# Performance work log

Measured on AMD Instinct MI355X. Metric: run time of the kernel, lower is better.

## Reference

```python
import jax, jax.numpy as jnp
import numpy as np

EPS = 1e-5
B, CIN, L = 512, 5, 1024   # batch, input channels, msp length == d_model
COUT, A, NB = 32, 13, 5    # CNN branch channels, max_atoms, num_bonds_prediction


def conv1d(x, w, pad, groups=1):
    # x: (N, C, L), w: (O, I/groups, K)
    return jax.lax.conv_general_dilated(
        x, w, window_strides=(1,), padding=[(pad, pad)],
        dimension_numbers=("NCH", "OIH", "NCH"), feature_group_count=groups)


def batchnorm(x, g, b):
    # training-mode BN over (N, L) per channel, as nn.BatchNorm1d in train()
    m = jnp.mean(x, axis=(0, 2), keepdims=True)
    v = jnp.var(x, axis=(0, 2), keepdims=True)
    return (x - m) * jax.lax.rsqrt(v + EPS) * g[None, :, None] + b[None, :, None]


def setup_inputs() -> dict:
    key = jax.random.key(0)
    ks = jax.random.split(key, 16)
    n = jax.random.normal
    inp = {
        "src": n(ks[0], (B, CIN, L), dtype=jnp.float32),
        "mask": jnp.ones((B, A), dtype=bool),
        "max_atoms": A,
        # CNN branch 1 (kernel 5) : depthwise, pointwise, BN, residual 1x1 conv
        "dw1": n(ks[1], (CIN, 1, 5), dtype=jnp.float32) * 0.2,
        "pw1": n(ks[2], (COUT, CIN, 1), dtype=jnp.float32) * 0.2,
        "g1": jnp.ones((COUT,), jnp.float32),
        "be1": jnp.zeros((COUT,), jnp.float32),
        "r1w": n(ks[3], (COUT, CIN, 1), dtype=jnp.float32) * 0.2,
        "r1b": jnp.zeros((COUT,), jnp.float32),
        # CNN branch 2 (kernel 3)
        "dw2": n(ks[4], (CIN, 1, 3), dtype=jnp.float32) * 0.2,
        "pw2": n(ks[5], (COUT, CIN, 1), dtype=jnp.float32) * 0.2,
        "g2": jnp.ones((COUT,), jnp.float32),
        "be2": jnp.zeros((COUT,), jnp.float32),
        "r2w": n(ks[6], (COUT, CIN, 1), dtype=jnp.float32) * 0.2,
        "r2b": jnp.zeros((COUT,), jnp.float32),
        # EdgeClassify2 linears: ll1 (2*COUT -> A), fl (2*L -> NB)
        "ll1w": n(ks[7], (A, 2 * COUT), dtype=jnp.float32) * 0.1,
        "ll1b": jnp.zeros((A,), jnp.float32),
        "flw": n(ks[8], (NB, 2 * L), dtype=jnp.float32) * 0.02,
        "flb": jnp.zeros((NB,), jnp.float32),
    }
    return inp


def reference(src, mask, max_atoms, dw1, pw1, g1, be1, r1w, r1b,
              dw2, pw2, g2, be2, r2w, r2b, ll1w, ll1b, flw, flb):
    # ---- CNN encoder ----
    e1 = jax.nn.relu(batchnorm(conv1d(conv1d(src, dw1, 2, groups=CIN), pw1, 0), g1, be1))
    e1 = e1 * (conv1d(src, r1w, 0) + r1b[None, :, None])
    e2 = jax.nn.relu(batchnorm(conv1d(conv1d(src, dw2, 1, groups=CIN), pw2, 0), g2, be2))
    e2 = e2 * (conv1d(src, r2w, 0) + r2b[None, :, None])
    x = jnp.concatenate([e1, e2], axis=1)          # (B, 2*COUT, L)
    # ---- EdgeClassify2 ----
    # ll1 over channel dim: (B, 2*COUT, L) -> (B, A, L)
    h = jnp.einsum("bcl,ac->bal", x, ll1w) + ll1b[None, :, None]
    # vectorized replacement of the O(A^2) python loop:
    # final_e[:, i, j] = concat(h[:, min(i,j)], h[:, max(i,j)])
    idx = jnp.arange(max_atoms)
    mn = jnp.minimum(idx[:, None], idx[None, :])   # (A, A)
    mx = jnp.maximum(idx[:, None], idx[None, :])
    final_e = jnp.concatenate([h[:, mn, :], h[:, mx, :]], axis=-1)  # (B, A, A, 2L)
    out = jnp.einsum("bijd,nd->bijn", final_e, flw) + flb           # (B, A, A, NB)
    return out
```

## Files before the change

kernel.cpp:

```cpp
#include <hip/hip_runtime.h>
#include <hip/hip_bf16.h>

#define BB 512
#define LL 1024
#define AA 13
#define NBP 5
#define NTOT (BB * LL)
#define EPSV 1e-5f

#define WS_F     192
#define WS_PART  256
#define WS_CONST 10496

typedef __attribute__((ext_vector_type(8))) short bhalf8;
typedef __attribute__((ext_vector_type(4))) float floatx4;

template<int CTRL, int RM, bool BC>
__device__ __forceinline__ float dppadd(float v) {
    int t = __builtin_amdgcn_update_dpp(0, __float_as_int(v), CTRL, RM, 0xf, BC);
    return v + __int_as_float(t);
}
__device__ __forceinline__ float wave_sum(float v) {
    v = dppadd<0x111, 0xf, true >(v);
    v = dppadd<0x112, 0xf, true >(v);
    v = dppadd<0x114, 0xf, true >(v);
    v = dppadd<0x118, 0xf, true >(v);
    v = dppadd<0x142, 0xa, false>(v);
    v = dppadd<0x143, 0xc, false>(v);
    return v;
}

__global__ __launch_bounds__(256) void k_moments(
    const float* __restrict__ src,
    const float* __restrict__ dw1,
    const float* __restrict__ dw2,
    const float* __restrict__ flw,
    float* __restrict__ ws)
{
    __shared__ float red[4][40];
    __shared__ float fred[4];
    int tid = threadIdx.x;
    int gid = blockIdx.x * 256 + tid;
    int b = gid >> 7, L0 = (gid & 127) << 3;
    const float* sb = src + b * (5 * LL);

    float w1[5][5], w2[5][3];
#pragma unroll
    for (int c = 0; c < 5; c++) {
#pragma unroll
        for (int t = 0; t < 5; t++) w1[c][t] = dw1[c*5+t];
#pragma unroll
        for (int t = 0; t < 3; t++) w2[c][t] = dw2[c*3+t];
    }

    float x[5][16];
#pragma unroll
    for (int c5 = 0; c5 < 5; c5++) {
        const float* sp = sb + c5 * LL;
        float4 xa = (L0 >= 4)    ? *(const float4*)(sp + L0 - 4) : make_float4(0,0,0,0);
        float4 xb = *(const float4*)(sp + L0);
        float4 xc = *(const float4*)(sp + L0 + 4);
        float4 xd = (L0 <= 1012) ? *(const float4*)(sp + L0 + 8) : make_float4(0,0,0,0);
        x[c5][0]=xa.x; x[c5][1]=xa.y; x[c5][2]=xa.z; x[c5][3]=xa.w;
        x[c5][4]=xb.x; x[c5][5]=xb.y; x[c5][6]=xb.z; x[c5][7]=xb.w;
        x[c5][8]=xc.x; x[c5][9]=xc.y; x[c5][10]=xc.z; x[c5][11]=xc.w;
        x[c5][12]=xd.x; x[c5][13]=xd.y; x[c5][14]=xd.z; x[c5][15]=xd.w;
    }

    float acc[40];
#pragma unroll
    for (int k = 0; k < 40; k++) acc[k] = 0.f;

#pragma unroll
    for (int k = 0; k < 8; k++) {
        float d1[5], d2[5];
#pragma unroll
        for (int c5 = 0; c5 < 5; c5++) {
            d1[c5] = w1[c5][0]*x[c5][k+2] + w1[c5][1]*x[c5][k+3] + w1[c5][2]*x[c5][k+4]
                   + w1[c5][3]*x[c5][k+5] + w1[c5][4]*x[c5][k+6];
            d2[c5] = w2[c5][0]*x[c5][k+3] + w2[c5][1]*x[c5][k+4] + w2[c5][2]*x[c5][k+5];
        }
#pragma unroll
        for (int j = 0; j < 5; j++) { acc[j] += d1[j]; acc[20+j] += d2[j]; }
#pragma unroll
        for (int j = 0; j < 5; j++)
#pragma unroll
            for (int kk = j; kk < 5; kk++) {
                int idx = j*(11-j)/2 + (kk - j);
                acc[5+idx]  += d1[j]*d1[kk];
                acc[25+idx] += d2[j]*d2[kk];
            }
    }

    int lane = tid & 63, wv = tid >> 6;
#pragma unroll
    for (int k = 0; k < 40; k++) acc[k] = wave_sum(acc[k]);
    if (lane == 63) {
#pragma unroll
        for (int k = 0; k < 40; k++) red[wv][k] = acc[k];
    }
    __syncthreads();
    if (tid < 40) {
        ws[WS_PART + blockIdx.x * 40 + tid] =
            red[0][tid] + red[1][tid] + red[2][tid] + red[3][tid];
    }

    if (blockIdx.x < 10) {
        int nn = blockIdx.x;
        int n = nn < 5 ? nn : nn - 5;
        int off = nn < 5 ? 0 : LL;
        float4 v = *(const float4*)(flw + n * (2*LL) + off + tid * 4);
        float s = wave_sum(v.x + v.y + v.z + v.w);
        if (lane == 63) fred[wv] = s;
        __syncthreads();
        if (tid == 0) ws[WS_F + nn] = fred[0] + fred[1] + fred[2] + fred[3];
    }
}

__global__ __launch_bounds__(320) void k_prep(
    float* __restrict__ ws,
    const float* __restrict__ pw1, const float* __restrict__ pw2,
    const float* __restrict__ g1,  const float* __restrict__ be1,
    const float* __restrict__ g2,  const float* __restrict__ be2,
    const float* __restrict__ r1w, const float* __restrict__ r2w,
    const float* __restrict__ r1b, const float* __restrict__ r2b)
{
    __shared__ float momS[40];
    int tid = threadIdx.x;
    {
        int k = tid >> 3, sub = tid & 7;
        float v = 0.f;
#pragma unroll 8
        for (int t2 = 0; t2 < 32; t2++) v += ws[WS_PART + (sub + (t2 << 3)) * 40 + k];
        v += __shfl_xor(v, 1, 64);
        v += __shfl_xor(v, 2, 64);
        v += __shfl_xor(v, 4, 64);
        if (sub == 0) momS[k] = v;
    }
    __syncthreads();
    if (tid < 64) {
        int brc = tid >> 5, o = tid & 31;
        const float invN = 1.0f / (float)NTOT;
        const float* pw = brc ? pw2 : pw1;
        const float* rw = brc ? r2w : r1w;
        const float* s  = momS + (brc ? 20 : 0);
        const float* M  = momS + (brc ? 25 : 5);
        float pwv[5], rwv[5], md[5];
#pragma unroll
        for (int j = 0; j < 5; j++) { pwv[j] = pw[o*5+j]; rwv[j] = rw[o*5+j]; md[j] = s[j] * invN; }
        float meanY = 0.f;
#pragma unroll
        for (int j = 0; j < 5; j++) meanY += pwv[j] * md[j];
        float ey2 = 0.f;
#pragma unroll
        for (int j = 0; j < 5; j++)
#pragma unroll
            for (int k = 0; k < 5; k++) {
                int lo = j < k ? j : k, hi = j < k ? k : j;
                int idx = lo*(11-lo)/2 + (hi - lo);
                ey2 += pwv[j] * pwv[k] * (M[idx] * invN);
            }
        float varY = ey2 - meanY * meanY;
        if (varY < 0.f) varY = 0.f;
        float gg = brc ? g2[o] : g1[o];
        float bb = brc ? be2[o] : be1[o];
        float rb = brc ? r2b[o] : r1b[o];
        float sc = gg * rsqrtf(varY + EPSV);
        float sh = bb - meanY * sc;
        float* dst = ws + WS_CONST + tid * 16;
        dst[0] = pwv[0]*sc; dst[1] = pwv[1]*sc; dst[2] = pwv[2]*sc; dst[3] = pwv[3]*sc;
        dst[4] = pwv[4]*sc; dst[5] = sh;        dst[6] = rb;        dst[7] = 0.f;
        dst[8] = rwv[0];    dst[9] = rwv[1];    dst[10] = rwv[2];   dst[11] = rwv[3];
        dst[12] = rwv[4];   dst[13] = 0.f;      dst[14] = 0.f;      dst[15] = 0.f;
    }
}

__global__ __launch_bounds__(512, 4) void k_fused(
    const float* __restrict__ src,
    const float* __restrict__ dw1,
    const float* __restrict__ dw2,
    const float* __restrict__ flw,
    const float* __restrict__ ll1w,
    const float* __restrict__ ll1b,
    const float* __restrict__ flb,
    const float* __restrict__ ws,
    float* __restrict__ out)
{
    __shared__ float llT[832];
    __shared__ __align__(16) unsigned int eBuf[8192];

    int tid = threadIdx.x, b = blockIdx.x;
    int lane = tid & 63;
    int gu = __builtin_amdgcn_readfirstlane(tid >> 6);
    int br = gu >> 2;
    int c0 = gu << 3;

    const float* srcB = src + b * (5 * LL);

    for (int idx = tid; idx < 832; idx += 512) {
        int cc = idx / 13, a = idx - cc * 13;
        llT[idx] = ll1w[a * 64 + cc];
    }

    float wdw[5][5];
    if (br == 0) {
#pragma unroll
        for (int c5 = 0; c5 < 5; c5++)
#pragma unroll
            for (int t = 0; t < 5; t++) wdw[c5][t] = dw1[c5*5+t];
    } else {
#pragma unroll
        for (int c5 = 0; c5 < 5; c5++) {
            wdw[c5][0] = 0.f;
            wdw[c5][1] = dw2[c5*3+0]; wdw[c5][2] = dw2[c5*3+1]; wdw[c5][3] = dw2[c5*3+2];
            wdw[c5][4] = 0.f;
        }
    }
    const float* cb = ws + WS_CONST + (c0 << 4);

    int mt   = gu & 3;
    int kgrp = gu >> 2;
    floatx4 Cacc = {0.f, 0.f, 0.f, 0.f};

    int nB = lane & 15;
    int kg = (lane >> 4) << 3;
    const float* fbase = flw + (nB % 5) * 2048 + (nB / 5) * 1024;

    char* eb = (char*)eBuf;

#pragma unroll 1
    for (int p = 0; p < 8; ++p) {
        float fv[2][8];
        {
            int gl0 = (p << 7) + (kgrp << 6) + kg;
            if (nB < 10) {
                float4 a0 = *(const float4*)(fbase + gl0);
                float4 a1 = *(const float4*)(fbase + gl0 + 4);
                float4 b0 = *(const float4*)(fbase + gl0 + 32);
                float4 b1 = *(const float4*)(fbase + gl0 + 36);
                fv[0][0]=a0.x; fv[0][1]=a0.y; fv[0][2]=a0.z; fv[0][3]=a0.w;
                fv[0][4]=a1.x; fv[0][5]=a1.y; fv[0][6]=a1.z; fv[0][7]=a1.w;
                fv[1][0]=b0.x; fv[1][1]=b0.y; fv[1][2]=b0.z; fv[1][3]=b0.w;
                fv[1][4]=b1.x; fv[1][5]=b1.y; fv[1][6]=b1.z; fv[1][7]=b1.w;
            } else {
#pragma unroll
                for (int j = 0; j < 8; j++) { fv[0][j] = 0.f; fv[1][j] = 0.f; }
            }
        }

        int l0 = (p << 7) + (lane << 1);
        float dv[5][2], sv[5][2];
#pragma unroll
        for (int c5 = 0; c5 < 5; c5++) {
            const float* s5 = srcB + (c5 << 10);
            float2 xa = (l0 >= 2)    ? *(const float2*)(s5 + l0 - 2) : make_float2(0.f, 0.f);
            float2 xb = *(const float2*)(s5 + l0);
            float2 xc = (l0 <= 1020) ? *(const float2*)(s5 + l0 + 2) : make_float2(0.f, 0.f);
            float xx[6] = {xa.x, xa.y, xb.x, xb.y, xc.x, xc.y};
            sv[c5][0] = xb.x; sv[c5][1] = xb.y;
            if (br == 0) {
#pragma unroll
                for (int q = 0; q < 2; q++)
                    dv[c5][q] = wdw[c5][0]*xx[q] + wdw[c5][1]*xx[q+1] + wdw[c5][2]*xx[q+2]
                              + wdw[c5][3]*xx[q+3] + wdw[c5][4]*xx[q+4];
            } else {
#pragma unroll
                for (int q = 0; q < 2; q++)
                    dv[c5][q] = wdw[c5][1]*xx[q+1] + wdw[c5][2]*xx[q+2] + wdw[c5][3]*xx[q+3];
            }
        }

        int wcol = lane << 2;
#pragma unroll
        for (int ci = 0; ci < 8; ci++) {
            const float4 A  = *(const float4*)(cb + ci*16);
            const float4 B2 = *(const float4*)(cb + ci*16 + 4);
            const float4 R0 = *(const float4*)(cb + ci*16 + 8);
            const float4 R1 = *(const float4*)(cb + ci*16 + 12);
            unsigned int hw[2], lw[2];
#pragma unroll
            for (int q = 0; q < 2; q++) {
                float y = B2.y + A.x*dv[0][q] + A.y*dv[1][q] + A.z*dv[2][q]
                                + A.w*dv[3][q] + B2.x*dv[4][q];
                float r = B2.z + R0.x*sv[0][q] + R0.y*sv[1][q] + R0.z*sv[2][q]
                                + R0.w*sv[3][q] + R1.x*sv[4][q];
                float e = fmaxf(y, 0.f) * r;
                unsigned int u = __float_as_uint(e);
                hw[q] = u & 0xFFFF0000u;
                float lf = e - __uint_as_float(hw[q]);
                lw[q] = __float_as_uint(lf) & 0xFFFF0000u;
            }
            int c = c0 + ci;
            int off = (c << 8) + (wcol ^ ((c & 7) << 4));
            *(unsigned int*)(eb + off)         = (hw[0] >> 16) | hw[1];
            *(unsigned int*)(eb + 16384 + off) = (lw[0] >> 16) | lw[1];
        }
        __syncthreads();

        {
            int arow = (mt << 4) + (lane & 15);
            int swz  = (arow & 7) << 4;
            int rb2  = arow << 8;
            bhalf8 bH[2], bL[2];
#pragma unroll
            for (int kk = 0; kk < 2; kk++)
#pragma unroll
                for (int j = 0; j < 8; j++) {
                    float f = fv[kk][j];
                    unsigned int u = __float_as_uint(f);
                    bH[kk][j] = (short)(u >> 16);
                    float lf = f - __uint_as_float(u & 0xFFFF0000u);
                    bL[kk][j] = (short)(__float_as_uint(lf) >> 16);
                }
#pragma unroll
            for (int kk = 0; kk < 2; kk++) {
                int kbyte = (((kgrp << 6) + (kk << 5) + kg) << 1) ^ swz;
                bhalf8 aH = *(const bhalf8*)(eb + rb2 + kbyte);
                bhalf8 aL = *(const bhalf8*)(eb + 16384 + rb2 + kbyte);
                Cacc = __builtin_amdgcn_mfma_f32_16x16x32_bf16(aH, bH[kk], Cacc, 0, 0, 0);
                Cacc = __builtin_amdgcn_mfma_f32_16x16x32_bf16(aH, bL[kk], Cacc, 0, 0, 0);
                Cacc = __builtin_amdgcn_mfma_f32_16x16x32_bf16(aL, bH[kk], Cacc, 0, 0, 0);
            }
        }
        __syncthreads();
    }

    {
        float* part = (float*)eBuf;
        int basep = (gu << 8) + ((lane >> 4) << 6) + (lane & 15);
        part[basep]      = Cacc[0];
        part[basep + 16] = Cacc[1];
        part[basep + 32] = Cacc[2];
        part[basep + 48] = Cacc[3];
    }
    __syncthreads();
    float* SarrF = (float*)eBuf + 4096;
    for (int idx = tid; idx < 1024; idx += 512) {
        int c = idx >> 4, n = idx & 15;
        int mt2 = c >> 4, row = c & 15;
        const float* part = (const float*)eBuf;
        int o = (row << 4) + n;
        SarrF[idx] = part[mt2 * 256 + o] + part[(4 + mt2) * 256 + o];
    }
    __syncthreads();

    float* PQ = (float*)eBuf + 5120;
    if (tid < 130) {
        int half = tid >= 65 ? 1 : 0;
        int q = tid - half * 65;
        int a = q / 5, n = q - a * 5;
        int col = half * 5 + n;
        float v = ll1b[a] * ws[WS_F + col];
#pragma unroll 8
        for (int cc = 0; cc < 64; cc++) v += llT[cc * 13 + a] * SarrF[(cc << 4) + col];
        PQ[tid] = v;
    }
    __syncthreads();

    for (int idx = tid; idx < AA * AA * NBP; idx += 512) {
        int i = idx / 65;
        int rr = idx - i * 65;
        int j = rr / 5, n = rr - j * 5;
        int mn = i < j ? i : j, mx = i < j ? j : i;
        out[b * (AA * AA * NBP) + idx] = PQ[mn * 5 + n] + PQ[65 + mx * 5 + n] + flb[n];
    }
}

extern "C" void kernel_launch(void* const* d_in, const int* in_sizes, int n_in,
                              void* d_out, int out_size, void* d_ws, size_t ws_size,
                              hipStream_t stream) {
    const float* src  = (const float*)d_in[0];
    const float* dw1  = (const float*)d_in[3];
    const float* pw1  = (const float*)d_in[4];
    const float* g1   = (const float*)d_in[5];
    const float* be1  = (const float*)d_in[6];
    const float* r1w  = (const float*)d_in[7];
    const float* r1b  = (const float*)d_in[8];
    const float* dw2  = (const float*)d_in[9];
    const float* pw2  = (const float*)d_in[10];
    const float* g2   = (const float*)d_in[11];
    const float* be2  = (const float*)d_in[12];
    const float* r2w  = (const float*)d_in[13];
    const float* r2b  = (const float*)d_in[14];
    const float* ll1w = (const float*)d_in[15];
    const float* ll1b = (const float*)d_in[16];
    const float* flw  = (const float*)d_in[17];
    const float* flb  = (const float*)d_in[18];
    float* ws  = (float*)d_ws;
    float* out = (float*)d_out;

    k_moments<<<256, 256, 0, stream>>>(src, dw1, dw2, flw, ws);
    k_prep<<<1, 320, 0, stream>>>(ws, pw1, pw2, g1, be1, g2, be2, r1w, r2w, r1b, r2b);
    k_fused<<<BB, 512, 0, stream>>>(src, dw1, dw2, flw, ll1w, ll1b, flb, ws, out);
}
```

Baseline: 153.0 us.

## Split fused kernel across L halves and add separate output epilogue kernel

The main fused kernel now launches two blocks per batch element, each covering half of the sequence length. Each block writes its partial 64x10 contraction to workspace, and a new k_out kernel sums the two halves and applies ll1 and the pairwise output expansion. This doubles the block count to fill more compute units on the GPU, at the cost of an extra kernel launch and a workspace round trip. Separately, the bf16 hi/lo split now uses packed round-to-nearest conversion instead of manual truncation.

```diff
diff --git a/kernel.cpp b/kernel.cpp
--- a/kernel.cpp
+++ b/kernel.cpp
@@ -11,9 +11,16 @@
 #define WS_F     192
 #define WS_PART  256
 #define WS_CONST 10496
+#define WS_S     16384
 
 typedef __attribute__((ext_vector_type(8))) short bhalf8;
 typedef __attribute__((ext_vector_type(4))) float floatx4;
+
+__device__ __forceinline__ unsigned int pk_bf16(float a, float b) {
+    __hip_bfloat162 h = __float22bfloat162_rn(make_float2(a, b));
+    union { __hip_bfloat162 h2; unsigned int u; } cv; cv.h2 = h;
+    return cv.u;
+}
 
 template<int CTRL, int RM, bool BC>
 __device__ __forceinline__ float dppadd(float v) {
@@ -180,16 +187,13 @@
     const float* __restrict__ dw1,
     const float* __restrict__ dw2,
     const float* __restrict__ flw,
-    const float* __restrict__ ll1w,
-    const float* __restrict__ ll1b,
-    const float* __restrict__ flb,
-    const float* __restrict__ ws,
-    float* __restrict__ out)
+    const float* __restrict__ ws_ro,
+    float* __restrict__ ws)
 {
-    __shared__ float llT[832];
     __shared__ __align__(16) unsigned int eBuf[8192];
 
-    int tid = threadIdx.x, b = blockIdx.x;
+    int tid = threadIdx.x, bb = blockIdx.x;
+    int b = bb >> 1, h = bb & 1;
     int lane = tid & 63;
     int gu = __builtin_amdgcn_readfirstlane(tid >> 6);
     int br = gu >> 2;
@@ -197,11 +201,6 @@
 
     const float* srcB = src + b * (5 * LL);
 
-    for (int idx = tid; idx < 832; idx += 512) {
-        int cc = idx / 13, a = idx - cc * 13;
-        llT[idx] = ll1w[a * 64 + cc];
-    }
-
     float wdw[5][5];
     if (br == 0) {
 #pragma unroll
@@ -216,7 +215,7 @@
             wdw[c5][4] = 0.f;
         }
     }
-    const float* cb = ws + WS_CONST + (c0 << 4);
+    const float* cb = ws_ro + WS_CONST + (c0 << 4);
 
     int mt   = gu & 3;
     int kgrp = gu >> 2;
@@ -229,10 +228,10 @@
     char* eb = (char*)eBuf;
 
 #pragma unroll 1
-    for (int p = 0; p < 8; ++p) {
+    for (int p = 0; p < 4; ++p) {
         float fv[2][8];
         {
-            int gl0 = (p << 7) + (kgrp << 6) + kg;
+            int gl0 = (h << 9) + (p << 7) + (kgrp << 6) + kg;
             if (nB < 10) {
                 float4 a0 = *(const float4*)(fbase + gl0);
                 float4 a1 = *(const float4*)(fbase + gl0 + 4);
@@ -248,7 +247,7 @@
             }
         }
 
-        int l0 = (p << 7) + (lane << 1);
+        int l0 = (h << 9) + (p << 7) + (lane << 1);
         float dv[5][2], sv[5][2];
 #pragma unroll
         for (int c5 = 0; c5 < 5; c5++) {
@@ -277,23 +276,23 @@
             const float4 B2 = *(const float4*)(cb + ci*16 + 4);
             const float4 R0 = *(const float4*)(cb + ci*16 + 8);
             const float4 R1 = *(const float4*)(cb + ci*16 + 12);
-            unsigned int hw[2], lw[2];
+            float e[2];
 #pragma unroll
             for (int q = 0; q < 2; q++) {
                 float y = B2.y + A.x*dv[0][q] + A.y*dv[1][q] + A.z*dv[2][q]
                                 + A.w*dv[3][q] + B2.x*dv[4][q];
                 float r = B2.z + R0.x*sv[0][q] + R0.y*sv[1][q] + R0.z*sv[2][q]
                                 + R0.w*sv[3][q] + R1.x*sv[4][q];
-                float e = fmaxf(y, 0.f) * r;
-                unsigned int u = __float_as_uint(e);
-                hw[q] = u & 0xFFFF0000u;
-                float lf = e - __uint_as_float(hw[q]);
-                lw[q] = __float_as_uint(lf) & 0xFFFF0000u;
-            }
+                e[q] = fmaxf(y, 0.f) * r;
+            }
+            unsigned int hp = pk_bf16(e[0], e[1]);
+            float hi0 = __uint_as_float(hp << 16);
+            float hi1 = __uint_as_float(hp & 0xFFFF0000u);
+            unsigned int lp = pk_bf16(e[0] - hi0, e[1] - hi1);
             int c = c0 + ci;
             int off = (c << 8) + (wcol ^ ((c & 7) << 4));
-            *(unsigned int*)(eb + off)         = (hw[0] >> 16) | hw[1];
-            *(unsigned int*)(eb + 16384 + off) = (lw[0] >> 16) | lw[1];
+            *(unsigned int*)(eb + off)         = hp;
+            *(unsigned int*)(eb + 16384 + off) = lp;
         }
         __syncthreads();
 
@@ -303,15 +302,19 @@
             int rb2  = arow << 8;
             bhalf8 bH[2], bL[2];
 #pragma unroll
-            for (int kk = 0; kk < 2; kk++)
-#pragma unroll
-                for (int j = 0; j < 8; j++) {
-                    float f = fv[kk][j];
-                    unsigned int u = __float_as_uint(f);
-                    bH[kk][j] = (short)(u >> 16);
-                    float lf = f - __uint_as_float(u & 0xFFFF0000u);
-                    bL[kk][j] = (short)(__float_as_uint(lf) >> 16);
+            for (int kk = 0; kk < 2; kk++) {
+                union { unsigned int u[4]; bhalf8 v; } uh, ul;
+#pragma unroll
+                for (int j = 0; j < 4; j++) {
+                    float f0 = fv[kk][2*j], f1 = fv[kk][2*j+1];
+                    unsigned int hp = pk_bf16(f0, f1);
+                    float hi0 = __uint_as_float(hp << 16);
+                    float hi1 = __uint_as_float(hp & 0xFFFF0000u);
+                    uh.u[j] = hp;
+                    ul.u[j] = pk_bf16(f0 - hi0, f1 - hi1);
                 }
+                bH[kk] = uh.v; bL[kk] = ul.v;
+            }
 #pragma unroll
             for (int kk = 0; kk < 2; kk++) {
                 int kbyte = (((kgrp << 6) + (kk << 5) + kg) << 1) ^ swz;
@@ -334,17 +337,36 @@
         part[basep + 48] = Cacc[3];
     }
     __syncthreads();
-    float* SarrF = (float*)eBuf + 4096;
-    for (int idx = tid; idx < 1024; idx += 512) {
-        int c = idx >> 4, n = idx & 15;
+    for (int idx = tid; idx < 640; idx += 512) {
+        int c = idx / 10, n = idx - c * 10;
         int mt2 = c >> 4, row = c & 15;
         const float* part = (const float*)eBuf;
         int o = (row << 4) + n;
-        SarrF[idx] = part[mt2 * 256 + o] + part[(4 + mt2) * 256 + o];
-    }
+        ws[WS_S + bb * 640 + idx] = part[mt2 * 256 + o] + part[(4 + mt2) * 256 + o];
+    }
+}
+
+__global__ __launch_bounds__(256) void k_out(
+    const float* __restrict__ ws,
+    const float* __restrict__ ll1w,
+    const float* __restrict__ ll1b,
+    const float* __restrict__ flb,
+    float* __restrict__ out)
+{
+    __shared__ float llT[832];
+    __shared__ float S[640];
+    __shared__ float PQ[130];
+
+    int tid = threadIdx.x, b = blockIdx.x;
+    for (int idx = tid; idx < 832; idx += 256) {
+        int cc = idx / 13, a = idx - cc * 13;
+        llT[idx] = ll1w[a * 64 + cc];
+    }
+    const float* s0 = ws + WS_S + (b * 2) * 640;
+    const float* s1 = ws + WS_S + (b * 2 + 1) * 640;
+    for (int idx = tid; idx < 640; idx += 256) S[idx] = s0[idx] + s1[idx];
     __syncthreads();
 
-    float* PQ = (float*)eBuf + 5120;
     if (tid < 130) {
         int half = tid >= 65 ? 1 : 0;
         int q = tid - half * 65;
@@ -352,12 +374,12 @@
         int col = half * 5 + n;
         float v = ll1b[a] * ws[WS_F + col];
 #pragma unroll 8
-        for (int cc = 0; cc < 64; cc++) v += llT[cc * 13 + a] * SarrF[(cc << 4) + col];
+        for (int cc = 0; cc < 64; cc++) v += llT[cc * 13 + a] * S[cc * 10 + col];
         PQ[tid] = v;
     }
     __syncthreads();
 
-    for (int idx = tid; idx < AA * AA * NBP; idx += 512) {
+    for (int idx = tid; idx < AA * AA * NBP; idx += 256) {
         int i = idx / 65;
         int rr = idx - i * 65;
         int j = rr / 5, n = rr - j * 5;
@@ -391,5 +413,6 @@
 
     k_moments<<<256, 256, 0, stream>>>(src, dw1, dw2, flw, ws);
     k_prep<<<1, 320, 0, stream>>>(ws, pw1, pw2, g1, be1, g2, be2, r1w, r2w, r1b, r2b);
-    k_fused<<<BB, 512, 0, stream>>>(src, dw1, dw2, flw, ll1w, ll1b, flb, ws, out);
-}
+    k_fused<<<BB * 2, 512, 0, stream>>>(src, dw1, dw2, flw, ws, ws);
+    k_out<<<BB, 256, 0, stream>>>(ws, ll1w, ll1b, flb, out);
+}
```

After: 157.5 us. 3.0% more time.
